# Kernel tuning notes

Hardware: AMD Instinct MI355X
Metric: run time of the kernel (lower is better)

The kernel has to match this reference:

```python
import jax, jax.numpy as jnp
import numpy as np

K_BINS = 8192
HIDDEN = 2048
SQRT2 = 1.4142135623730951
LEAKY_SLOPE = 0.01
TMIN = 1e-10


def setup_inputs() -> dict:
    key = jax.random.key(0)
    k0, k1, k2 = jax.random.split(key, 3)
    D = 2 * K_BINS  # mu length so that cat([mu, t]) has 2K+1 features
    # positive mu keeps mu ** (gamma - 1/(1-gamma)) (a fractional power) finite
    mu = jax.random.uniform(k0, (D,), jnp.float32, 0.1, 1.0)
    t = jnp.array([0.5], jnp.float32)
    gamma = jnp.array([0.5], jnp.float32)  # 1/(1-gamma) = 2 -> integral exponent
    W1 = jax.random.normal(k1, (D + 1, HIDDEN), jnp.float32) * (1.0 / np.sqrt(D + 1))
    b1 = jnp.zeros((HIDDEN,), jnp.float32)
    W2 = jax.random.normal(k2, (HIDDEN, D), jnp.float32) * (1.0 / np.sqrt(HIDDEN))
    b2 = jnp.zeros((D,), jnp.float32)
    return {"mu": mu, "t": t, "gamma": gamma, "W1": W1, "b1": b1,
            "W2": W2, "b2": b2, "K": K_BINS}


def reference(mu, t, gamma, W1, b1, W2, b2, K):
    g = gamma[0]
    # --- NN(cat([mu, t])) -> (mu_epsilon, ln_sigma_epsilon), each [K] ---
    inp = jnp.concatenate([mu, t])                      # [2K+1]
    h = jax.nn.leaky_relu(inp @ W1 + b1, LEAKY_SLOPE)   # [hidden]
    out = h @ W2 + b2                                   # [2K]
    mu_eps, ln_sig = out[:K], out[K:]
    # --- mu_x / sigma_x (t < tmin branch folded in via where) ---
    p_mu = g - 1.0 / (1.0 - g)
    p_eps = 1.0 / (1.0 - g)
    mu_x_nn = jnp.power(mu[:K], p_mu) * jnp.power(mu_eps, p_eps)
    sigma_x_nn = jnp.power(1.0 - g, -0.5) * jnp.exp(0.5 * ln_sig)
    use_nn = t[0] >= TMIN
    mu_x = jnp.where(use_nn, mu_x_nn, jnp.zeros_like(mu_eps))     # [K]
    sigma_x = jnp.where(use_nn, sigma_x_nn, jnp.ones_like(mu_eps))  # [K]
    # --- vectorized discretised CDF differences over the (D_out, K) grid ---
    kk = jnp.arange(K, dtype=jnp.float32)
    kl = 2.0 * (kk - 1.0) / (K - 1.0)   # left bin edges  [K]
    kr = 2.0 * kk / (K - 1.0)           # right bin edges [K]

    def cdf(x):  # x: [K] edges -> G: [D_out, K]
        z = (x[None, :] - mu_x[:, None]) / (sigma_x[:, None] * SQRT2)
        F = 0.5 * (1.0 + jax.lax.erf(z))
        return jnp.where(x[None, :] <= -1.0, 0.0,
                         jnp.where(x[None, :] >= 1.0, 1.0, F))

    return cdf(kr) - cdf(kl)  # [K, K] per-bin probabilities
```

## Files before the change

### kernel.cpp

```cpp
#include <hip/hip_runtime.h>
#include <math.h>

#define KBINS 8192
#define DDIM  16384
#define HID   2048
#define LASTROW 16384

#define C1 32
#define NB1 512
#define C2 32
#define NB2 64

static constexpr float SQRT2_F = 1.4142135623730951f;

__device__ __forceinline__ float fast_erff(float x) {
    float ax = fabsf(x);
    float t  = 1.0f / fmaf(0.3275911f, ax, 1.0f);
    float p  = t * (0.254829592f +
               t * (-0.284496736f +
               t * (1.421413741f +
               t * (-1.453152027f +
               t * 1.061405429f))));
    float r = 1.0f - p * __expf(-ax * ax);
    return copysignf(r, x);
}

__global__ void __launch_bounds__(256)
mv1_partial(const float* __restrict__ mu, const float* __restrict__ W1,
            float* __restrict__ part1) {
    __shared__ float a_s[C1];
    int r0 = blockIdx.y * C1;
    if (threadIdx.x < C1) a_s[threadIdx.x] = mu[r0 + threadIdx.x];
    __syncthreads();
    int c0 = (blockIdx.x * 256 + threadIdx.x) * 4;
    float4 acc = {0.f, 0.f, 0.f, 0.f};
    const float* wp = W1 + (size_t)r0 * HID + c0;
#pragma unroll 8
    for (int k = 0; k < C1; ++k) {
        float a = a_s[k];
        const float4 w = *reinterpret_cast<const float4*>(wp + (size_t)k * HID);
        acc.x += a * w.x; acc.y += a * w.y; acc.z += a * w.z; acc.w += a * w.w;
    }
    *reinterpret_cast<float4*>(part1 + (size_t)blockIdx.y * HID + c0) = acc;
}

__global__ void __launch_bounds__(256)
h_reduce(const float* __restrict__ part1, const float* __restrict__ b1,
         const float* __restrict__ W1, const float* __restrict__ t,
         float* __restrict__ h) {
    __shared__ float red[4][64];
    int lane = threadIdx.x & 63;
    int sub  = threadIdx.x >> 6;
    int col  = blockIdx.x * 64 + lane;
    float s = 0.f;
    for (int rb = sub; rb < NB1; rb += 4)
        s += part1[(size_t)rb * HID + col];
    red[sub][lane] = s;
    __syncthreads();
    if (threadIdx.x < 64) {
        int c = blockIdx.x * 64 + threadIdx.x;
        float v = b1[c] + t[0] * W1[(size_t)LASTROW * HID + c];
        v += red[0][threadIdx.x] + red[1][threadIdx.x]
           + red[2][threadIdx.x] + red[3][threadIdx.x];
        h[c] = (v >= 0.f) ? v : 0.01f * v;
    }
}

__global__ void __launch_bounds__(256)
mv2_partial(const float* __restrict__ h, const float* __restrict__ W2,
            float* __restrict__ part2) {
    __shared__ float hs[C2];
    int r0 = blockIdx.y * C2;
    if (threadIdx.x < C2) hs[threadIdx.x] = h[r0 + threadIdx.x];
    __syncthreads();
    int c0 = (blockIdx.x * 256 + threadIdx.x) * 4;
    float4 acc = {0.f, 0.f, 0.f, 0.f};
    const float* wp = W2 + (size_t)r0 * DDIM + c0;
#pragma unroll 8
    for (int k = 0; k < C2; ++k) {
        float a = hs[k];
        const float4 w = *reinterpret_cast<const float4*>(wp + (size_t)k * DDIM);
        acc.x += a * w.x; acc.y += a * w.y; acc.z += a * w.z; acc.w += a * w.w;
    }
    *reinterpret_cast<float4*>(part2 + (size_t)blockIdx.y * DDIM + c0) = acc;
}

__global__ void __launch_bounds__(256)
scalars(const float* __restrict__ part2, const float* __restrict__ b2,
        const float* __restrict__ mu, const float* __restrict__ t,
        const float* __restrict__ gamma,
        float* __restrict__ mu_x, float* __restrict__ sigma_x) {
    int i = blockIdx.x * 256 + threadIdx.x;
    float s0 = b2[i];
    float s1 = b2[i + KBINS];
    for (int rb = 0; rb < NB2; ++rb) {
        s0 += part2[(size_t)rb * DDIM + i];
        s1 += part2[(size_t)rb * DDIM + i + KBINS];
    }
    float g  = gamma[0];
    float pe = 1.0f / (1.0f - g);
    float pm = g - pe;
    bool use_nn = (t[0] >= 1e-10f);
    float mx = powf(mu[i], pm) * powf(s0, pe);
    float sx = powf(1.0f - g, -0.5f) * expf(0.5f * s1);
    mu_x[i]    = use_nn ? mx : 0.0f;
    sigma_x[i] = use_nn ? sx : 1.0f;
}

__global__ void __launch_bounds__(256)
cdf_row(const float* __restrict__ mu_x, const float* __restrict__ sigma_x,
        float* __restrict__ out) {
    int i   = blockIdx.x;
    int tid = threadIdx.x;
    float m   = mu_x[i];
    float inv = 1.0f / (sigma_x[i] * SQRT2_F);
    const float sc = 2.0f / 8191.0f;
    float* orow = out + (size_t)i * KBINS;
#pragma unroll
    for (int it = 0; it < 8; ++it) {
        int j0 = it * 1024 + tid * 4;
        float4 r;
        if (j0 > 4096) {
            r.x = r.y = r.z = r.w = 0.f;
        } else {
            float F[5];
#pragma unroll
            for (int k = 0; k < 5; ++k) {
                float x = (float)(j0 - 1 + k) * sc;
                float f;
                if (x >= 1.0f)       f = 1.0f;
                else if (x <= -1.0f) f = 0.0f;
                else                 f = 0.5f * (1.0f + fast_erff((x - m) * inv));
                F[k] = f;
            }
            r.x = F[1] - F[0]; r.y = F[2] - F[1]; r.z = F[3] - F[2]; r.w = F[4] - F[3];
        }
        *reinterpret_cast<float4*>(orow + j0) = r;
    }
}

extern "C" void kernel_launch(void* const* d_in, const int* in_sizes, int n_in,
                              void* d_out, int out_size, void* d_ws, size_t ws_size,
                              hipStream_t stream) {
    const float* mu    = (const float*)d_in[0];
    const float* t     = (const float*)d_in[1];
    const float* gamma = (const float*)d_in[2];
    const float* W1    = (const float*)d_in[3];
    const float* b1    = (const float*)d_in[4];
    const float* W2    = (const float*)d_in[5];
    const float* b2    = (const float*)d_in[6];
    float* out = (float*)d_out;

    float* ws      = (float*)d_ws;
    float* part1   = ws;
    float* h       = part1 + (size_t)NB1 * HID;
    float* part2   = h + HID;
    float* mu_x    = part2 + (size_t)NB2 * DDIM;
    float* sigma_x = mu_x + KBINS;

    mv1_partial<<<dim3(2, NB1),  dim3(256), 0, stream>>>(mu, W1, part1);
    h_reduce   <<<dim3(32),      dim3(256), 0, stream>>>(part1, b1, W1, t, h);
    mv2_partial<<<dim3(16, NB2), dim3(256), 0, stream>>>(h, W2, part2);
    scalars    <<<dim3(32),      dim3(256), 0, stream>>>(part2, b2, mu, t, gamma, mu_x, sigma_x);
    cdf_row    <<<dim3(KBINS),   dim3(256), 0, stream>>>(mu_x, sigma_x, out);
}
```

Measured before the change: 166.2 us.

## Replace erf CDF differences with midpoint Gaussian density and split matvec accumulators

The CDF-difference kernel stops evaluating erf at both bin edges. For interior bins it now computes the Gaussian density at the bin midpoint times the bin width, using one exp per output with precomputed affine coefficients. Only the final bin before x=1 keeps an explicit erf tail. The two matvec kernels use two independent accumulators per thread with full unrolling, and the reduction loops get unroll pragmas. The midpoint rule is an approximation whose accuracy depends on sigma being large relative to the bin width, so results can drift from the reference for small sigma.

```diff
diff --git a/kernel.cpp b/kernel.cpp
--- a/kernel.cpp
+++ b/kernel.cpp
@@ -11,7 +11,8 @@
 #define C2 32
 #define NB2 64
 
-static constexpr float SQRT2_F = 1.4142135623730951f;
+static constexpr float SQRT2_F  = 1.4142135623730951f;
+static constexpr float INVSQ2PI = 0.3989422804014327f;
 
 __device__ __forceinline__ float fast_erff(float x) {
     float ax = fabsf(x);
@@ -33,14 +34,19 @@
     if (threadIdx.x < C1) a_s[threadIdx.x] = mu[r0 + threadIdx.x];
     __syncthreads();
     int c0 = (blockIdx.x * 256 + threadIdx.x) * 4;
-    float4 acc = {0.f, 0.f, 0.f, 0.f};
+    float4 acc0 = {0.f, 0.f, 0.f, 0.f};
+    float4 acc1 = {0.f, 0.f, 0.f, 0.f};
     const float* wp = W1 + (size_t)r0 * HID + c0;
-#pragma unroll 8
-    for (int k = 0; k < C1; ++k) {
-        float a = a_s[k];
-        const float4 w = *reinterpret_cast<const float4*>(wp + (size_t)k * HID);
-        acc.x += a * w.x; acc.y += a * w.y; acc.z += a * w.z; acc.w += a * w.w;
+#pragma unroll
+    for (int k = 0; k < C1; k += 2) {
+        float a0 = a_s[k];
+        float a1 = a_s[k + 1];
+        const float4 w0 = *reinterpret_cast<const float4*>(wp + (size_t)k * HID);
+        const float4 w1 = *reinterpret_cast<const float4*>(wp + (size_t)(k + 1) * HID);
+        acc0.x += a0 * w0.x; acc0.y += a0 * w0.y; acc0.z += a0 * w0.z; acc0.w += a0 * w0.w;
+        acc1.x += a1 * w1.x; acc1.y += a1 * w1.y; acc1.z += a1 * w1.z; acc1.w += a1 * w1.w;
     }
+    float4 acc = {acc0.x + acc1.x, acc0.y + acc1.y, acc0.z + acc1.z, acc0.w + acc1.w};
     *reinterpret_cast<float4*>(part1 + (size_t)blockIdx.y * HID + c0) = acc;
 }
 
@@ -53,6 +59,7 @@
     int sub  = threadIdx.x >> 6;
     int col  = blockIdx.x * 64 + lane;
     float s = 0.f;
+#pragma unroll 8
     for (int rb = sub; rb < NB1; rb += 4)
         s += part1[(size_t)rb * HID + col];
     red[sub][lane] = s;
@@ -74,14 +81,19 @@
     if (threadIdx.x < C2) hs[threadIdx.x] = h[r0 + threadIdx.x];
     __syncthreads();
     int c0 = (blockIdx.x * 256 + threadIdx.x) * 4;
-    float4 acc = {0.f, 0.f, 0.f, 0.f};
+    float4 acc0 = {0.f, 0.f, 0.f, 0.f};
+    float4 acc1 = {0.f, 0.f, 0.f, 0.f};
     const float* wp = W2 + (size_t)r0 * DDIM + c0;
-#pragma unroll 8
-    for (int k = 0; k < C2; ++k) {
-        float a = hs[k];
-        const float4 w = *reinterpret_cast<const float4*>(wp + (size_t)k * DDIM);
-        acc.x += a * w.x; acc.y += a * w.y; acc.z += a * w.z; acc.w += a * w.w;
+#pragma unroll
+    for (int k = 0; k < C2; k += 2) {
+        float a0 = hs[k];
+        float a1 = hs[k + 1];
+        const float4 w0 = *reinterpret_cast<const float4*>(wp + (size_t)k * DDIM);
+        const float4 w1 = *reinterpret_cast<const float4*>(wp + (size_t)(k + 1) * DDIM);
+        acc0.x += a0 * w0.x; acc0.y += a0 * w0.y; acc0.z += a0 * w0.z; acc0.w += a0 * w0.w;
+        acc1.x += a1 * w1.x; acc1.y += a1 * w1.y; acc1.z += a1 * w1.z; acc1.w += a1 * w1.w;
     }
+    float4 acc = {acc0.x + acc1.x, acc0.y + acc1.y, acc0.z + acc1.z, acc0.w + acc1.w};
     *reinterpret_cast<float4*>(part2 + (size_t)blockIdx.y * DDIM + c0) = acc;
 }
 
@@ -93,6 +105,7 @@
     int i = blockIdx.x * 256 + threadIdx.x;
     float s0 = b2[i];
     float s1 = b2[i + KBINS];
+#pragma unroll 8
     for (int rb = 0; rb < NB2; ++rb) {
         s0 += part2[(size_t)rb * DDIM + i];
         s1 += part2[(size_t)rb * DDIM + i + KBINS];
@@ -112,28 +125,32 @@
         float* __restrict__ out) {
     int i   = blockIdx.x;
     int tid = threadIdx.x;
-    float m   = mu_x[i];
-    float inv = 1.0f / (sigma_x[i] * SQRT2_F);
+    float m    = mu_x[i];
+    float invs = 1.0f / sigma_x[i];
     const float sc = 2.0f / 8191.0f;
+    float A    = sc * invs;
+    float B    = (-1.0f / 8191.0f - m) * invs;
+    float coef = INVSQ2PI * A;
     float* orow = out + (size_t)i * KBINS;
 #pragma unroll
     for (int it = 0; it < 8; ++it) {
         int j0 = it * 1024 + tid * 4;
         float4 r;
-        if (j0 > 4096) {
+        if (j0 < 4096) {
+            float u0 = fmaf((float)(j0 + 0), A, B);
+            float u1 = fmaf((float)(j0 + 1), A, B);
+            float u2 = fmaf((float)(j0 + 2), A, B);
+            float u3 = fmaf((float)(j0 + 3), A, B);
+            r.x = coef * __expf(-0.5f * u0 * u0);
+            r.y = coef * __expf(-0.5f * u1 * u1);
+            r.z = coef * __expf(-0.5f * u2 * u2);
+            r.w = coef * __expf(-0.5f * u3 * u3);
+        } else if (j0 == 4096) {
+            float z = (8190.0f / 8191.0f - m) * invs * (1.0f / SQRT2_F);
+            r.x = 0.5f * (1.0f - fast_erff(z));
+            r.y = r.z = r.w = 0.f;
+        } else {
             r.x = r.y = r.z = r.w = 0.f;
-        } else {
-            float F[5];
-#pragma unroll
-            for (int k = 0; k < 5; ++k) {
-                float x = (float)(j0 - 1 + k) * sc;
-                float f;
-                if (x >= 1.0f)       f = 1.0f;
-                else if (x <= -1.0f) f = 0.0f;
-                else                 f = 0.5f * (1.0f + fast_erff((x - m) * inv));
-                F[k] = f;
-            }
-            r.x = F[1] - F[0]; r.y = F[2] - F[1]; r.z = F[3] - F[2]; r.w = F[4] - F[3];
         }
         *reinterpret_cast<float4*>(orow + j0) = r;
     }
```

Measured after the change: 147.8 us. 11.1% less time.
